# Optimization experiments

Measured on AMD Instinct MI355X. Metric: run time of the kernel, lower is better.

Reference implementation:

```python
import jax, jax.numpy as jnp
import numpy as np

B, S, D, H = 2, 2048, 1024, 16
HD = D // H
EPS = 1e-8
LN_EPS = 1e-5


def setup_inputs() -> dict:
    key = jax.random.key(0)
    ks = jax.random.split(key, 12)
    std = 0.02
    inp = {}
    inp["x"] = jax.random.normal(ks[0], (B, S, D), jnp.float32)
    # q/k/v/out projections (stored (in, out); y = x @ W + b)
    inp["Wq"] = jax.random.normal(ks[1], (D, D), jnp.float32) * std
    inp["bq"] = jnp.zeros((D,), jnp.float32)
    inp["Wk"] = jax.random.normal(ks[2], (D, D), jnp.float32) * std
    inp["bk"] = jnp.zeros((D,), jnp.float32)
    inp["Wv"] = jax.random.normal(ks[3], (D, D), jnp.float32) * std
    inp["bv"] = jnp.zeros((D,), jnp.float32)
    inp["Wo"] = jax.random.normal(ks[4], (D, D), jnp.float32) * std
    inp["bo"] = jnp.zeros((D,), jnp.float32)
    # 4 DeltaResidualBlocks stacked on axis 0: [q, k, v, out]
    inp["dWk"] = jax.random.normal(ks[5], (4, D, D), jnp.float32) * 0.01  # k_proj, no bias
    inp["dbw"] = jnp.zeros((4, D), jnp.float32)                           # beta_proj weight (init zeros)
    inp["dbb"] = jnp.full((4,), -4.0, jnp.float32)                        # beta_proj bias
    inp["dWv"] = jax.random.normal(ks[6], (4, D), jnp.float32) * 0.02     # v_proj weight (d_v=1)
    inp["dbv"] = jnp.zeros((4,), jnp.float32)                             # v_proj bias
    inp["ln_g"] = jnp.ones((D,), jnp.float32)
    inp["ln_b"] = jnp.zeros((D,), jnp.float32)
    return inp


def reference(x, Wq, bq, Wk, bk, Wv, bv, Wo, bo, dWk, dbw, dbb, dWv, dbv, ln_g, ln_b):
    def delta(h, v_in, i):
        # DeltaResidualBlock (d_v=1): h + beta * k * (v - k.h)
        k_raw = jnp.einsum('bsd,de->bse', h, dWk[i])
        k = k_raw / (jnp.linalg.norm(k_raw, axis=-1, keepdims=True) + EPS)
        beta = 2.0 * jax.nn.sigmoid(jnp.einsum('bsd,d->bs', h, dbw[i])[..., None] + dbb[i])  # (B,S,1)
        v = jnp.einsum('bsd,d->bs', v_in, dWv[i])[..., None] + dbv[i]                        # (B,S,1)
        k_dot_h = jnp.sum(k * h, axis=-1, keepdims=True)
        return h + beta * k * (v - k_dot_h)

    q = delta(x, x @ Wq + bq, 0)
    k = delta(x, x @ Wk + bk, 1)
    v = delta(x, x @ Wv + bv, 2)

    # (B,S,D) -> (B,H,S,HD)
    q = q.reshape(B, S, H, HD).transpose(0, 2, 1, 3)
    k = k.reshape(B, S, H, HD).transpose(0, 2, 1, 3)
    v = v.reshape(B, S, H, HD).transpose(0, 2, 1, 3)

    scale = HD ** -0.5
    scores = jnp.einsum('bhqd,bhkd->bhqk', q, k) * scale
    attn = jax.nn.softmax(scores, axis=-1)
    out = jnp.einsum('bhqk,bhkd->bhqd', attn, v)
    out = out.transpose(0, 2, 1, 3).reshape(B, S, D)
    out = out @ Wo + bo

    y = delta(x, out, 3)

    # LayerNorm
    mu = jnp.mean(y, axis=-1, keepdims=True)
    var = jnp.mean((y - mu) ** 2, axis=-1, keepdims=True)
    y = (y - mu) / jnp.sqrt(var + LN_EPS) * ln_g + ln_b
    return y
```

## Files before the change

### kernel.cpp

```cpp
#include <hip/hip_runtime.h>

#define BB 2
#define SS 2048
#define DD 1024
#define HH 16
#define HD 64
#define MM (BB*SS)
#define KC 4
#define KT_PER (SS/64/KC)
#define NTT 16
#define KSTEPS (DD/64)

typedef unsigned short u16;
typedef __attribute__((ext_vector_type(8))) short bf16x8;
typedef __attribute__((ext_vector_type(4))) float f32x4;

typedef __attribute__((address_space(1))) const unsigned int* gas_t;
typedef __attribute__((address_space(3))) unsigned int* las_t;

#ifndef __has_builtin
#define __has_builtin(x) 0
#endif
#if __has_builtin(__builtin_amdgcn_exp2f)
#define EXP2F(x) __builtin_amdgcn_exp2f(x)
#else
#define EXP2F(x) __expf((x)*0.6931471805599453f)
#endif
#define QSCALE 0.18033688011112042f

__device__ __forceinline__ void gl_lds16(const u16* g, u16* l){
  __builtin_amdgcn_global_load_lds((gas_t)g, (las_t)l, 16, 0, 0);
}

__device__ __forceinline__ u16 f2bf(float f){
  unsigned u = __float_as_uint(f);
  u += 0x7FFF + ((u >> 16) & 1);
  return (u16)(u >> 16);
}
__device__ __forceinline__ float bf2f(u16 h){
  return __uint_as_float(((unsigned)h) << 16);
}
__device__ __forceinline__ float dot4f(float4 a, float4 b){
  return a.x*b.x + a.y*b.y + a.z*b.z + a.w*b.w;
}

template <int CTRL>
__device__ __forceinline__ float dppadd(float x){
  int y = __builtin_amdgcn_update_dpp(0, __float_as_int(x), CTRL, 0xF, 0xF, true);
  return x + __int_as_float(y);
}
__device__ __forceinline__ float4 wsum64_f4(float4 v){
  #define DPP_ST(c) v.x=dppadd<c>(v.x); v.y=dppadd<c>(v.y); v.z=dppadd<c>(v.z); v.w=dppadd<c>(v.w);
  DPP_ST(0x111) DPP_ST(0x112) DPP_ST(0x114) DPP_ST(0x118) DPP_ST(0x142) DPP_ST(0x143)
  #undef DPP_ST
  return v;
}
__device__ __forceinline__ float2 wsum64_f2(float2 v){
  #define DPP_ST(c) v.x=dppadd<c>(v.x); v.y=dppadd<c>(v.y);
  DPP_ST(0x111) DPP_ST(0x112) DPP_ST(0x114) DPP_ST(0x118) DPP_ST(0x142) DPP_ST(0x143)
  #undef DPP_ST
  return v;
}

#define SB0() __builtin_amdgcn_sched_barrier(0)
#define SBAR() do { \
  __builtin_amdgcn_sched_barrier(0); \
  __builtin_amdgcn_s_barrier(); \
  __builtin_amdgcn_sched_barrier(0); \
} while (0)

#define NB_CONV 2048
#define NB_TRAN 1024
#define NB_PREC 4100
#define NB_PREP (NB_CONV+NB_TRAN+NB_PREC)
__global__ void prep_kernel(const float* __restrict__ x, u16* __restrict__ xb,
                            const float* __restrict__ dWk, u16* __restrict__ dWkT,
                            const float* __restrict__ Wq_, const float* __restrict__ bq_,
                            const float* __restrict__ Wk_, const float* __restrict__ bk_,
                            const float* __restrict__ Wv_, const float* __restrict__ bv_,
                            const float* __restrict__ Wo_, const float* __restrict__ bo_,
                            const float* __restrict__ dWv, const float* __restrict__ dbv,
                            float* __restrict__ wv, float* __restrict__ cv) {
  int blk = blockIdx.x, t = threadIdx.x;
  if (blk < NB_CONV) {
    size_t idx = ((size_t)blk*256 + t)*8;
    float4 a = *(const float4*)(x + idx);
    float4 b = *(const float4*)(x + idx + 4);
    union { u16 u[8]; uint4 v; } pk;
    pk.u[0]=f2bf(a.x); pk.u[1]=f2bf(a.y); pk.u[2]=f2bf(a.z); pk.u[3]=f2bf(a.w);
    pk.u[4]=f2bf(b.x); pk.u[5]=f2bf(b.y); pk.u[6]=f2bf(b.z); pk.u[7]=f2bf(b.w);
    *(uint4*)(xb + idx) = pk.v;
    return;
  }
  blk -= NB_CONV;
  if (blk < NB_TRAN) {
    int i = blk >> 8, rest = blk & 255;
    int k0 = (rest >> 4) << 6, n0 = (rest & 15) << 6;
    const float* src = dWk + (size_t)i*DD*DD;
    u16* dst = dWkT + (size_t)i*DD*DD;
    __shared__ u16 tr[64*68];
    const int krb = (t >> 4) << 2;
    const int nqb = (t & 15) << 2;
    float4 v0 = *(const float4*)(src + (size_t)(k0+krb+0)*DD + n0 + nqb);
    float4 v1 = *(const float4*)(src + (size_t)(k0+krb+1)*DD + n0 + nqb);
    float4 v2 = *(const float4*)(src + (size_t)(k0+krb+2)*DD + n0 + nqb);
    float4 v3 = *(const float4*)(src + (size_t)(k0+krb+3)*DD + n0 + nqb);
    *(uint2*)(&tr[(nqb+0)*68 + krb]) = make_uint2(
        (unsigned)f2bf(v0.x) | ((unsigned)f2bf(v1.x)<<16),
        (unsigned)f2bf(v2.x) | ((unsigned)f2bf(v3.x)<<16));
    *(uint2*)(&tr[(nqb+1)*68 + krb]) = make_uint2(
        (unsigned)f2bf(v0.y) | ((unsigned)f2bf(v1.y)<<16),
        (unsigned)f2bf(v2.y) | ((unsigned)f2bf(v3.y)<<16));
    *(uint2*)(&tr[(nqb+2)*68 + krb]) = make_uint2(
        (unsigned)f2bf(v0.z) | ((unsigned)f2bf(v1.z)<<16),
        (unsigned)f2bf(v2.z) | ((unsigned)f2bf(v3.z)<<16));
    *(uint2*)(&tr[(nqb+3)*68 + krb]) = make_uint2(
        (unsigned)f2bf(v0.w) | ((unsigned)f2bf(v1.w)<<16),
        (unsigned)f2bf(v2.w) | ((unsigned)f2bf(v3.w)<<16));
    __syncthreads();
    const int n = t >> 2, c = t & 3;
    uint2 r0 = *(uint2*)(&tr[n*68 + c*16 + 0]);
    uint2 r1 = *(uint2*)(&tr[n*68 + c*16 + 4]);
    uint2 r2 = *(uint2*)(&tr[n*68 + c*16 + 8]);
    uint2 r3 = *(uint2*)(&tr[n*68 + c*16 + 12]);
    u16* dp = dst + (size_t)(n0+n)*DD + k0 + c*16;
    *(uint4*)(dp + 0) = make_uint4(r0.x, r0.y, r1.x, r1.y);
    *(uint4*)(dp + 8) = make_uint4(r2.x, r2.y, r3.x, r3.y);
    return;
  }
  blk -= NB_TRAN;
  {
    int i = blk / 1025, row = blk % 1025;
    const float* W    = (i==0)?Wq_:(i==1)?Wk_:(i==2)?Wv_:Wo_;
    const float* bvec = (i==0)?bq_:(i==1)?bk_:(i==2)?bv_:bo_;
    const float* s = dWv + i*DD;
    __shared__ float red[256];
    float acc = 0.f;
    if (row < DD) {
      const float* r = W + (size_t)row * DD;
      for (int e = t; e < DD; e += 256) acc += r[e]*s[e];
    } else {
      for (int e = t; e < DD; e += 256) acc += bvec[e]*s[e];
    }
    red[t] = acc; __syncthreads();
    for (int off=128; off>0; off>>=1){ if(t<off) red[t]+=red[t+off]; __syncthreads(); }
    if (t==0) {
      if (row < DD) wv[i*DD + row] = red[0];
      else          cv[i] = red[0] + dbv[i];
    }
  }
}

__device__ __forceinline__ void stage_half(const u16* __restrict__ g, u16* l,
                                           int k0, int half, int isA,
                                           int wid, int lane) {
  const int lr = lane>>3, lc = lane&7;
  #pragma unroll
  for (int j=0; j<2; j++) {
    const int u = wid*2 + j;
    int grow;
    if (isA) grow = ((u & 8) ? 128 + ((u & 7)<<3) : (u<<3)) + (half<<6);
    else     grow = ((u>>2)<<6) + ((u&3)<<3) + (half<<5);
    gl_lds16(g + (size_t)(grow + lr)*DD + k0 + ((lc^lr)<<3), l + grow*64);
  }
}

__device__ __forceinline__ void lda4(const u16* base, int row0, int q15, int quad,
                                     int sw, bf16x8 (&f)[4][2]) {
  #pragma unroll
  for (int mf=0; mf<4; mf++)
    #pragma unroll
    for (int kk=0; kk<2; kk++)
      f[mf][kk] = *(const bf16x8*)(base + (row0 + mf*16 + q15)*64 + (((kk*4+quad)^sw)<<3));
}
__device__ __forceinline__ void ldb2(const u16* base, int row0, int q15, int quad,
                                     int sw, bf16x8 (&f)[2][2]) {
  #pragma unroll
  for (int nf=0; nf<2; nf++)
    #pragma unroll
    for (int kk=0; kk<2; kk++)
      f[nf][kk] = *(const bf16x8*)(base + (row0 + nf*16 + q15)*64 + (((kk*4+quad)^sw)<<3));
}
__device__ __forceinline__ void quad_mfma(const bf16x8 (&af)[4][2], const bf16x8 (&bfr)[2][2],
                                          f32x4 (&acc)[8][4], int mo, int no) {
  __builtin_amdgcn_s_setprio(1);
  #pragma unroll
  for (int kk=0; kk<2; kk++)
    #pragma unroll
    for (int mf=0; mf<4; mf++)
      #pragma unroll
      for (int nf=0; nf<2; nf++)
        acc[mo+mf][no+nf] = __builtin_amdgcn_mfma_f32_16x16x32_bf16(
            bfr[nf][kk], af[mf][kk], acc[mo+mf][no+nf], 0,0,0);
  __builtin_amdgcn_s_setprio(0);
}

__global__ __launch_bounds__(512, 2) void gemm_dwk_8ph(const u16* __restrict__ xb,
                          const u16* __restrict__ Bt, u16* __restrict__ kraw) {
  const int bid = blockIdx.x;
  const int xcd = bid & 7, rr = bid >> 3;
  const int i = xcd >> 1;
  const int mt = ((xcd & 1) << 3) | (rr & 7);
  const int ntile = rr >> 3;
  const int m0 = mt << 8, n0 = ntile << 8;
  const u16* Ab = xb + (size_t)m0*DD;
  const u16* Bb = Bt + (size_t)i*DD*DD + (size_t)n0*DD;
  u16* C = kraw + (size_t)i*MM*DD;

  const int t = threadIdx.x, wid = t>>6, lane = t&63;
  const int q15 = lane&15, quad = lane>>4, sw = q15&7;
  const int wm = wid>>2, wn = wid&3;
  const int arow = wm<<7, brow = wn<<6;

  __shared__ u16 As[2][256*64];
  __shared__ u16 Bs[2][256*64];

  f32x4 acc[8][4];
  #pragma unroll
  for (int a=0;a<8;a++)
    #pragma unroll
    for (int b2=0;b2<4;b2++) acc[a][b2] = (f32x4){0.f,0.f,0.f,0.f};

  stage_half(Ab, As[0], 0,  0, 1, wid, lane);
  stage_half(Bb, Bs[0], 0,  0, 0, wid, lane);
  stage_half(Bb, Bs[0], 0,  1, 0, wid, lane);
  stage_half(Ab, As[0], 0,  1, 1, wid, lane);
  stage_half(Ab, As[1], 64, 0, 1, wid, lane);
  stage_half(Bb, Bs[1], 64, 0, 0, wid, lane);
  stage_half(Bb, Bs[1], 64, 1, 0, wid, lane);
  SB0();
  asm volatile("s_waitcnt vmcnt(6)" ::: "memory");
  SBAR();

  for (int u=0; u<KSTEPS; ++u) {
    const int cur = u & 1;
    const u16* Ac = As[cur]; const u16* Bc = Bs[cur];
    const int k1 = (u+1 < KSTEPS ? u+1 : KSTEPS-1) << 6;
    const int k2 = (u+2 < KSTEPS ? u+2 : KSTEPS-1) << 6;
    bf16x8 a0[4][2], a1[4][2], b0[2][2], b1[2][2];

    lda4(Ac, arow,    q15, quad, sw, a0);
    ldb2(Bc, brow,    q15, quad, sw, b0);
    ldb2(Bc, brow+32, q15, quad, sw, b1);
    stage_half(Ab, As[cur^1], k1, 1, 1, wid, lane);
    SB0();
    quad_mfma(a0, b0, acc, 0, 0);
    quad_mfma(a0, b1, acc, 0, 2);
    SB0();
    lda4(Ac, arow+64, q15, quad, sw, a1);
    SB0();
    __builtin_amdgcn_s_barrier();
    SB0();
    stage_half(Ab, As[cur], k2, 0, 1, wid, lane);
    stage_half(Bb, Bs[cur], k2, 0, 0, wid, lane);
    stage_half(Bb, Bs[cur], k2, 1, 0, wid, lane);
    SB0();
    quad_mfma(a1, b1, acc, 4, 2);
    quad_mfma(a1, b0, acc, 4, 0);
    SB0();
    asm volatile("s_waitcnt vmcnt(6)" ::: "memory");
    __builtin_amdgcn_s_barrier();
    SB0();
  }

  #pragma unroll
  for (int mf=0; mf<8; mf++) {
    const int m = m0 + arow + mf*16 + q15;
    u16* Crow = C + (size_t)m*DD + n0 + brow;
    #pragma unroll
    for (int nf=0; nf<4; nf++) {
      unsigned u0 = (unsigned)f2bf(acc[mf][nf][0]) | ((unsigned)f2bf(acc[mf][nf][1]) << 16);
      unsigned u1 = (unsigned)f2bf(acc[mf][nf][2]) | ((unsigned)f2bf(acc[mf][nf][3]) << 16);
      *(uint2*)(Crow + nf*16 + quad*4) = make_uint2(u0, u1);
    }
  }
}

__global__ void delta_qkv_kernel(const float* __restrict__ x, const u16* __restrict__ kraw,
                                 const float* __restrict__ dbw, const float* __restrict__ dbb,
                                 const float* __restrict__ wv, const float* __restrict__ cv,
                                 u16* __restrict__ qk, float* __restrict__ Vw) {
  int m = blockIdx.x, t = threadIdx.x, w = t>>6, lane = t&63;
  const float* xr = x + (size_t)m*DD;
  float4 xv = *(const float4*)(xr + t*4);
  __shared__ float4 part[3][4];
  float4 kvs[3];
  #pragma unroll
  for (int i=0;i<3;i++) {
    ushort4 ku = *(const ushort4*)(kraw + (size_t)i*MM*DD + (size_t)m*DD + t*4);
    float4 kv = make_float4(bf2f(ku.x), bf2f(ku.y), bf2f(ku.z), bf2f(ku.w));
    kvs[i] = kv;
    float4 bwv = *(const float4*)(dbw + i*DD + t*4);
    float4 wvv = *(const float4*)(wv  + i*DD + t*4);
    float4 red = make_float4(dot4f(kv,kv), dot4f(kv,xv), dot4f(xv,bwv), dot4f(xv,wvv));
    red = wsum64_f4(red);
    if (lane==63) part[i][w] = red;
  }
  __syncthreads();
  float cc[3];
  #pragma unroll
  for (int i=0;i<3;i++) {
    float4 r0=part[i][0], r1=part[i][1], r2=part[i][2], r3=part[i][3];
    float s0=r0.x+r1.x+r2.x+r3.x, s1=r0.y+r1.y+r2.y+r3.y;
    float s2=r0.z+r1.z+r2.z+r3.z, s3=r0.w+r1.w+r2.w+r3.w;
    float nrmE = sqrtf(s0) + 1e-8f;
    float kdh  = s1 / nrmE;
    float beta = 2.f / (1.f + __expf(-(s2 + dbb[i])));
    float vs   = s3 + cv[i];
    cc[i] = beta * (vs - kdh) / nrmE;
  }
  {
    float c = cc[0]; float4 kv = kvs[0];
    ushort4 ou;
    ou.x = f2bf((xv.x + c*kv.x)*QSCALE); ou.y = f2bf((xv.y + c*kv.y)*QSCALE);
    ou.z = f2bf((xv.z + c*kv.z)*QSCALE); ou.w = f2bf((xv.w + c*kv.w)*QSCALE);
    *(ushort4*)(qk + (size_t)m*DD + t*4) = ou;
  }
  {
    float c = cc[1]; float4 kv = kvs[1];
    ushort4 ou;
    ou.x = f2bf(xv.x + c*kv.x); ou.y = f2bf(xv.y + c*kv.y);
    ou.z = f2bf(xv.z + c*kv.z); ou.w = f2bf(xv.w + c*kv.w);
    *(ushort4*)(qk + (size_t)MM*DD + (size_t)m*DD + t*4) = ou;
  }
  {
    float c = cc[2]; float4 kv = kvs[2];
    float4 vv = make_float4(xv.x + c*kv.x, xv.y + c*kv.y, xv.z + c*kv.z, xv.w + c*kv.w);
    float4 w3 = *(const float4*)(wv + 3*DD + t*4);
    float s = dot4f(vv, w3);
    #pragma unroll
    for (int off=1; off<16; off<<=1) s += __shfl_xor(s, off);
    if ((lane & 15) == 0) {
      int head = t >> 4;
      int b = m >> 11, srow = m & (SS-1);
      Vw[((size_t)(b*HH + head))*SS + srow] = s;
    }
  }
}

__global__ __launch_bounds__(256, 6) void flash_mfma(const u16* __restrict__ qb,
     const u16* __restrict__ kb, const float* __restrict__ Vw,
     float* __restrict__ l_arr, float* __restrict__ pv_arr) {
  const int qt = blockIdx.x, h = blockIdx.y;
  const int b = blockIdx.z >> 2, kc = blockIdx.z & 3;
  const int t = threadIdx.x, w = t>>6, lane = t&63, q15 = lane&15, quad = lane>>4;
  const int sw = q15 & 7;
  __shared__ u16 Ks[3][32*64];
  __shared__ float Vws[KT_PER*64];
  const size_t hb = (size_t)h*HD;
  const u16* kbase = kb + (size_t)(b*SS + kc*KT_PER*64)*DD + hb;
  const float* vwb = Vw + (size_t)(b*HH + h)*SS + kc*KT_PER*64;
  const int srow = (w<<3) + (lane>>3), schunk = (lane&7) ^ (lane>>3);
  u16* sdst = &Ks[0][0] + (w<<3)*64;

  bf16x8 qf[2];
  {
    const u16* qrow = qb + (size_t)(b*SS + qt*64 + w*16 + q15)*DD + hb;
    qf[0] = *(const bf16x8*)(qrow + quad*8);
    qf[1] = *(const bf16x8*)(qrow + 32 + quad*8);
  }
  if (t < KT_PER*64/4) {
    float4 v = *(const float4*)(vwb + t*4);
    *(float4*)(&Vws[t*4]) = v;
  }
  gl_lds16(kbase + (size_t)(0*32 + srow)*DD + schunk*8, sdst + 0*32*64);
  gl_lds16(kbase + (size_t)(1*32 + srow)*DD + schunk*8, sdst + 1*32*64);
  float l_acc = 0.f, pv_acc = 0.f;
  __syncthreads();

  #pragma unroll
  for (int kt=0; kt<NTT; kt++) {
    if (kt+2 < NTT)
      gl_lds16(kbase + (size_t)((kt+2)*32 + srow)*DD + schunk*8,
               sdst + ((kt+2)%3)*32*64);
    const u16* Kt = &Ks[kt%3][0];
    f32x4 S0 = (f32x4){0.f,0.f,0.f,0.f}, S1 = (f32x4){0.f,0.f,0.f,0.f};
    #pragma unroll
    for (int kk=0; kk<2; kk++) {
      bf16x8 k0 = *(const bf16x8*)(Kt + (q15)*64      + (((kk*4+quad)^sw)<<3));
      bf16x8 k1 = *(const bf16x8*)(Kt + (16+q15)*64   + (((kk*4+quad)^sw)<<3));
      S0 = __builtin_amdgcn_mfma_f32_16x16x32_bf16(k0, qf[kk], S0, 0,0,0);
      S1 = __builtin_amdgcn_mfma_f32_16x16x32_bf16(k1, qf[kk], S1, 0,0,0);
    }
    float4 va0 = *(const float4*)(&Vws[kt*32 + quad*4]);
    float4 va1 = *(const float4*)(&Vws[kt*32 + 16 + quad*4]);
    {
      float p0 = EXP2F(fminf(S0[0], 30.f));
      float p1 = EXP2F(fminf(S0[1], 30.f));
      float p2 = EXP2F(fminf(S0[2], 30.f));
      float p3 = EXP2F(fminf(S0[3], 30.f));
      l_acc  += (p0 + p1) + (p2 + p3);
      pv_acc += p0*va0.x + p1*va0.y + p2*va0.z + p3*va0.w;
    }
    {
      float p0 = EXP2F(fminf(S1[0], 30.f));
      float p1 = EXP2F(fminf(S1[1], 30.f));
      float p2 = EXP2F(fminf(S1[2], 30.f));
      float p3 = EXP2F(fminf(S1[3], 30.f));
      l_acc  += (p0 + p1) + (p2 + p3);
      pv_acc += p0*va1.x + p1*va1.y + p2*va1.z + p3*va1.w;
    }
    if (kt < NTT-1) {
      __builtin_amdgcn_sched_barrier(0);
      if (kt+2 < NTT) asm volatile("s_waitcnt vmcnt(1)" ::: "memory");
      else            asm volatile("s_waitcnt vmcnt(0)" ::: "memory");
      __builtin_amdgcn_s_barrier();
      __builtin_amdgcn_sched_barrier(0);
    }
  }
  l_acc  += __shfl_xor(l_acc, 16);  l_acc  += __shfl_xor(l_acc, 32);
  pv_acc += __shfl_xor(pv_acc, 16); pv_acc += __shfl_xor(pv_acc, 32);
  if (quad == 0) {
    int tok = b*SS + qt*64 + w*16 + q15;
    size_t idx = ((size_t)kc*MM + tok)*HH + h;
    l_arr[idx]  = l_acc;
    pv_arr[idx] = pv_acc;
  }
}

__global__ void final_kernel(const float* __restrict__ x, const u16* __restrict__ kraw3,
                             const float* __restrict__ l_arr, const float* __restrict__ pv_arr,
                             const float* __restrict__ dbw, const float* __restrict__ dbb,
                             const float* __restrict__ cv,
                             const float* __restrict__ ln_g, const float* __restrict__ ln_b,
                             float* __restrict__ out) {
  int m = blockIdx.x, t = threadIdx.x, w = t>>6, lane = t&63;
  const float* xr = x     + (size_t)m*DD;
  const u16*   kr = kraw3 + (size_t)m*DD;
  float4 xv  = *(const float4*)(xr + t*4);
  ushort4 ku = *(const ushort4*)(kr + t*4);
  float4 kv  = make_float4(bf2f(ku.x), bf2f(ku.y), bf2f(ku.z), bf2f(ku.w));
  float4 bwv = *(const float4*)(dbw + 3*DD + t*4);
  __shared__ float4 part[4];
  __shared__ float2 part2[4];
  __shared__ float v3s;
  if (t < 16) {
    float lsum = 0.f, psum = 0.f;
    #pragma unroll
    for (int kc=0; kc<KC; kc++) {
      size_t idx = ((size_t)kc*MM + m)*HH + t;
      lsum += l_arr[idx];
      psum += pv_arr[idx];
    }
    float val = psum / lsum;
    #pragma unroll
    for (int off=1; off<16; off<<=1) val += __shfl_xor(val, off);
    if (t==0) v3s = val;
  }
  float4 red = make_float4(dot4f(kv,kv), dot4f(kv,xv), dot4f(xv,bwv), 0.f);
  red = wsum64_f4(red);
  if (lane==63) part[w] = red;
  __syncthreads();
  float4 r0=part[0], r1=part[1], r2=part[2], r3=part[3];
  float s0=r0.x+r1.x+r2.x+r3.x, s1=r0.y+r1.y+r2.y+r3.y, s2=r0.z+r1.z+r2.z+r3.z;
  float nrmE = sqrtf(s0) + 1e-8f;
  float kdh  = s1 / nrmE;
  float beta = 2.f / (1.f + __expf(-(s2 + dbb[3])));
  float v3   = v3s + cv[3];
  float c = beta * (v3 - kdh) / nrmE;
  float y0 = xv.x + c*kv.x, y1 = xv.y + c*kv.y, y2 = xv.z + c*kv.z, y3 = xv.w + c*kv.w;
  float2 rr = make_float2(y0+y1+y2+y3, y0*y0+y1*y1+y2*y2+y3*y3);
  rr = wsum64_f2(rr);
  if (lane==63) part2[w] = rr;
  __syncthreads();
  float ssum = part2[0].x+part2[1].x+part2[2].x+part2[3].x;
  float ssq  = part2[0].y+part2[1].y+part2[2].y+part2[3].y;
  float mu   = ssum * (1.f/DD);
  float var  = ssq * (1.f/DD) - mu*mu;
  float rstd = rsqrtf(var + 1e-5f);
  float4 g  = *(const float4*)(ln_g + t*4);
  float4 bb = *(const float4*)(ln_b + t*4);
  float4 ov;
  ov.x = (y0-mu)*rstd*g.x + bb.x;
  ov.y = (y1-mu)*rstd*g.y + bb.y;
  ov.z = (y2-mu)*rstd*g.z + bb.z;
  ov.w = (y3-mu)*rstd*g.w + bb.w;
  *(float4*)(out + (size_t)m*DD + t*4) = ov;
}

extern "C" void kernel_launch(void* const* d_in, const int* in_sizes, int n_in,
                              void* d_out, int out_size, void* d_ws, size_t ws_size,
                              hipStream_t stream) {
  const float* x    = (const float*)d_in[0];
  const float* Wq_  = (const float*)d_in[1];
  const float* bq_  = (const float*)d_in[2];
  const float* Wk_  = (const float*)d_in[3];
  const float* bk_  = (const float*)d_in[4];
  const float* Wv_  = (const float*)d_in[5];
  const float* bv_  = (const float*)d_in[6];
  const float* Wo_  = (const float*)d_in[7];
  const float* bo_  = (const float*)d_in[8];
  const float* dWk  = (const float*)d_in[9];
  const float* dbw  = (const float*)d_in[10];
  const float* dbb  = (const float*)d_in[11];
  const float* dWv  = (const float*)d_in[12];
  const float* dbv  = (const float*)d_in[13];
  const float* ln_g = (const float*)d_in[14];
  const float* ln_b = (const float*)d_in[15];
  float* out = (float*)d_out;
  char* WS = (char*)d_ws;

  float* wv     = (float*)WS;
  float* cv     = (float*)(WS + 16384);
  u16*   kraw   = (u16*)  (WS + 16640);
  u16*   qk     = (u16*)  (WS + 16640 + (size_t)4*MM*DD*2);
  u16*   dWkT   = (u16*)  (WS + 16640 + (size_t)6*MM*DD*2);
  u16*   xb     = (u16*)  (WS + 16640 + (size_t)6*MM*DD*2 + (size_t)4*DD*DD*2);
  char*  tail   = WS + 16640 + (size_t)6*MM*DD*2 + (size_t)8*DD*DD*2;
  float* Vw     = (float*)tail;
  float* l_arr  = (float*)(tail + (size_t)BB*HH*SS*4);
  float* pv_arr = (float*)(tail + (size_t)BB*HH*SS*4 + (size_t)KC*MM*HH*4);

  prep_kernel<<<NB_PREP, 256, 0, stream>>>(
      x, xb, dWk, dWkT, Wq_,bq_,Wk_,bk_,Wv_,bv_,Wo_,bo_, dWv, dbv, wv, cv);
  gemm_dwk_8ph<<<256, 512, 0, stream>>>(xb, dWkT, kraw);
  delta_qkv_kernel<<<MM, 256, 0, stream>>>(x, kraw, dbw, dbb, wv, cv, qk, Vw);
  flash_mfma<<<dim3(SS/64, HH, BB*KC), 256, 0, stream>>>(
      qk, qk + (size_t)MM*DD, Vw, l_arr, pv_arr);
  final_kernel<<<MM, 256, 0, stream>>>(x, kraw + 3*(size_t)MM*DD, l_arr, pv_arr,
                                       dbw, dbb, cv, ln_g, ln_b, out);
}
```

Measured before the change: 219.8 us.

## Process two 64-row query sub-tiles per flash block to reuse K tiles

Each flash_mfma block now handles 128 query rows, two sub-tiles of 64, instead of 64. Each K tile loaded into LDS and then into registers feeds twice as many MFMAs, and the grid shrinks by half in x. This halves K global and LDS traffic per query row. The cost is more registers (launch bounds lowered from 6 to 5 waves) and fewer blocks, so there is less parallelism to hide latency.

```diff
diff --git a/kernel.cpp b/kernel.cpp
--- a/kernel.cpp
+++ b/kernel.cpp
@@ -9,6 +9,7 @@
 #define KC 4
 #define KT_PER (SS/64/KC)
 #define NTT 16
+#define QB 128
 #define KSTEPS (DD/64)
 
 typedef unsigned short u16;
@@ -338,7 +339,7 @@
   }
 }
 
-__global__ __launch_bounds__(256, 6) void flash_mfma(const u16* __restrict__ qb,
+__global__ __launch_bounds__(256, 5) void flash_mfma(const u16* __restrict__ qb,
      const u16* __restrict__ kb, const float* __restrict__ Vw,
      float* __restrict__ l_arr, float* __restrict__ pv_arr) {
   const int qt = blockIdx.x, h = blockIdx.y;
@@ -353,11 +354,12 @@
   const int srow = (w<<3) + (lane>>3), schunk = (lane&7) ^ (lane>>3);
   u16* sdst = &Ks[0][0] + (w<<3)*64;
 
-  bf16x8 qf[2];
-  {
-    const u16* qrow = qb + (size_t)(b*SS + qt*64 + w*16 + q15)*DD + hb;
-    qf[0] = *(const bf16x8*)(qrow + quad*8);
-    qf[1] = *(const bf16x8*)(qrow + 32 + quad*8);
+  bf16x8 qf[2][2];
+  #pragma unroll
+  for (int qs=0; qs<2; qs++) {
+    const u16* qrow = qb + (size_t)(b*SS + qt*QB + qs*64 + w*16 + q15)*DD + hb;
+    qf[qs][0] = *(const bf16x8*)(qrow + quad*8);
+    qf[qs][1] = *(const bf16x8*)(qrow + 32 + quad*8);
   }
   if (t < KT_PER*64/4) {
     float4 v = *(const float4*)(vwb + t*4);
@@ -365,7 +367,7 @@
   }
   gl_lds16(kbase + (size_t)(0*32 + srow)*DD + schunk*8, sdst + 0*32*64);
   gl_lds16(kbase + (size_t)(1*32 + srow)*DD + schunk*8, sdst + 1*32*64);
-  float l_acc = 0.f, pv_acc = 0.f;
+  float l_acc[2] = {0.f,0.f}, pv_acc[2] = {0.f,0.f};
   __syncthreads();
 
   #pragma unroll
@@ -374,31 +376,38 @@
       gl_lds16(kbase + (size_t)((kt+2)*32 + srow)*DD + schunk*8,
                sdst + ((kt+2)%3)*32*64);
     const u16* Kt = &Ks[kt%3][0];
-    f32x4 S0 = (f32x4){0.f,0.f,0.f,0.f}, S1 = (f32x4){0.f,0.f,0.f,0.f};
+    bf16x8 kr0[2], kr1[2];
     #pragma unroll
     for (int kk=0; kk<2; kk++) {
-      bf16x8 k0 = *(const bf16x8*)(Kt + (q15)*64      + (((kk*4+quad)^sw)<<3));
-      bf16x8 k1 = *(const bf16x8*)(Kt + (16+q15)*64   + (((kk*4+quad)^sw)<<3));
-      S0 = __builtin_amdgcn_mfma_f32_16x16x32_bf16(k0, qf[kk], S0, 0,0,0);
-      S1 = __builtin_amdgcn_mfma_f32_16x16x32_bf16(k1, qf[kk], S1, 0,0,0);
+      kr0[kk] = *(const bf16x8*)(Kt + (q15)*64    + (((kk*4+quad)^sw)<<3));
+      kr1[kk] = *(const bf16x8*)(Kt + (16+q15)*64 + (((kk*4+quad)^sw)<<3));
     }
     float4 va0 = *(const float4*)(&Vws[kt*32 + quad*4]);
     float4 va1 = *(const float4*)(&Vws[kt*32 + 16 + quad*4]);
-    {
-      float p0 = EXP2F(fminf(S0[0], 30.f));
-      float p1 = EXP2F(fminf(S0[1], 30.f));
-      float p2 = EXP2F(fminf(S0[2], 30.f));
-      float p3 = EXP2F(fminf(S0[3], 30.f));
-      l_acc  += (p0 + p1) + (p2 + p3);
-      pv_acc += p0*va0.x + p1*va0.y + p2*va0.z + p3*va0.w;
-    }
-    {
-      float p0 = EXP2F(fminf(S1[0], 30.f));
-      float p1 = EXP2F(fminf(S1[1], 30.f));
-      float p2 = EXP2F(fminf(S1[2], 30.f));
-      float p3 = EXP2F(fminf(S1[3], 30.f));
-      l_acc  += (p0 + p1) + (p2 + p3);
-      pv_acc += p0*va1.x + p1*va1.y + p2*va1.z + p3*va1.w;
+    #pragma unroll
+    for (int qs=0; qs<2; qs++) {
+      f32x4 S0 = (f32x4){0.f,0.f,0.f,0.f}, S1 = (f32x4){0.f,0.f,0.f,0.f};
+      #pragma unroll
+      for (int kk=0; kk<2; kk++) {
+        S0 = __builtin_amdgcn_mfma_f32_16x16x32_bf16(kr0[kk], qf[qs][kk], S0, 0,0,0);
+        S1 = __builtin_amdgcn_mfma_f32_16x16x32_bf16(kr1[kk], qf[qs][kk], S1, 0,0,0);
+      }
+      {
+        float p0 = EXP2F(fminf(S0[0], 30.f));
+        float p1 = EXP2F(fminf(S0[1], 30.f));
+        float p2 = EXP2F(fminf(S0[2], 30.f));
+        float p3 = EXP2F(fminf(S0[3], 30.f));
+        l_acc[qs]  += (p0 + p1) + (p2 + p3);
+        pv_acc[qs] += p0*va0.x + p1*va0.y + p2*va0.z + p3*va0.w;
+      }
+      {
+        float p0 = EXP2F(fminf(S1[0], 30.f));
+        float p1 = EXP2F(fminf(S1[1], 30.f));
+        float p2 = EXP2F(fminf(S1[2], 30.f));
+        float p3 = EXP2F(fminf(S1[3], 30.f));
+        l_acc[qs]  += (p0 + p1) + (p2 + p3);
+        pv_acc[qs] += p0*va1.x + p1*va1.y + p2*va1.z + p3*va1.w;
+      }
     }
     if (kt < NTT-1) {
       __builtin_amdgcn_sched_barrier(0);
@@ -408,13 +417,19 @@
       __builtin_amdgcn_sched_barrier(0);
     }
   }
-  l_acc  += __shfl_xor(l_acc, 16);  l_acc  += __shfl_xor(l_acc, 32);
-  pv_acc += __shfl_xor(pv_acc, 16); pv_acc += __shfl_xor(pv_acc, 32);
+  #pragma unroll
+  for (int qs=0; qs<2; qs++) {
+    l_acc[qs]  += __shfl_xor(l_acc[qs], 16);  l_acc[qs]  += __shfl_xor(l_acc[qs], 32);
+    pv_acc[qs] += __shfl_xor(pv_acc[qs], 16); pv_acc[qs] += __shfl_xor(pv_acc[qs], 32);
+  }
   if (quad == 0) {
-    int tok = b*SS + qt*64 + w*16 + q15;
-    size_t idx = ((size_t)kc*MM + tok)*HH + h;
-    l_arr[idx]  = l_acc;
-    pv_arr[idx] = pv_acc;
+    #pragma unroll
+    for (int qs=0; qs<2; qs++) {
+      int tok = b*SS + qt*QB + qs*64 + w*16 + q15;
+      size_t idx = ((size_t)kc*MM + tok)*HH + h;
+      l_arr[idx]  = l_acc[qs];
+      pv_arr[idx] = pv_acc[qs];
+    }
   }
 }
 
@@ -515,7 +530,7 @@
       x, xb, dWk, dWkT, Wq_,bq_,Wk_,bk_,Wv_,bv_,Wo_,bo_, dWv, dbv, wv, cv);
   gemm_dwk_8ph<<<256, 512, 0, stream>>>(xb, dWkT, kraw);
   delta_qkv_kernel<<<MM, 256, 0, stream>>>(x, kraw, dbw, dbb, wv, cv, qk, Vw);
-  flash_mfma<<<dim3(SS/64, HH, BB*KC), 256, 0, stream>>>(
+  flash_mfma<<<dim3(SS/QB, HH, BB*KC), 256, 0, stream>>>(
       qk, qk + (size_t)MM*DD, Vw, l_arr, pv_arr);
   final_kernel<<<MM, 256, 0, stream>>>(x, kraw + 3*(size_t)MM*DD, l_arr, pv_arr,
                                        dbw, dbb, cv, ln_g, ln_b, out);
```

Result: no change. 217.3 us (-1.1%).
